# Optimization experiments

Measured on AMD Instinct MI355X. Metric: run time of the kernel, lower is better.

## Reference

```python
import math
import jax, jax.numpy as jnp
import numpy as np

B, S, D, H = 2, 2048, 1024, 16
HD = D // H

def setup_inputs() -> dict:
    key = jax.random.key(0)
    k1, k2, k3, k4, k5, k6 = jax.random.split(key, 6)
    q = jax.random.normal(k1, (B, S, D), dtype=jnp.float32)
    kv_mask = jax.random.bernoulli(k2, 0.95, (B, S))
    attn_mask = jax.random.bernoulli(k3, 0.95, (B, S, S))
    # nn.Linear(model_dim, 3*model_dim, bias=False): y = x @ W.T, W:[3D, D]
    W_all = jax.random.normal(k4, (3 * D, D), dtype=jnp.float32) / math.sqrt(D)
    W_out = jax.random.normal(k5, (D, D), dtype=jnp.float32) / math.sqrt(D)
    b_out = jax.random.normal(k6, (D,), dtype=jnp.float32) * 0.01
    return {"q": q, "kv_mask": kv_mask, "attn_mask": attn_mask,
            "W_all": W_all, "W_out": W_out, "b_out": b_out}

def reference(q, kv_mask, attn_mask, W_all, W_out, b_out):
    b, s, d = q.shape
    # merge_masks: kv_mask expanded over query dim, AND-ed with attn_mask, head dim added
    merged = (kv_mask[:, None, :] & attn_mask)[:, None, :, :]          # [b,1,s,s] bool
    # fused self-attn qkv projection
    qkv = q @ W_all.T                                                   # [b,s,3d]
    q_out, k_out, v_out = jnp.split(qkv, 3, axis=-1)
    reshape = lambda x: x.reshape(b, s, H, HD).transpose(0, 2, 1, 3)    # [b,h,s,hd]
    q_out, k_out, v_out = reshape(q_out), reshape(k_out), reshape(v_out)
    scores = jnp.einsum('bhqd,bhkd->bhqk', q_out, k_out) / math.sqrt(HD)
    scores = jnp.where(merged, scores, -jnp.inf)                        # masked_fill(~mask, -inf)
    att = jax.nn.softmax(scores, axis=-1)
    att = jnp.nan_to_num(att)                                           # fully-masked rows -> 0
    a_out = jnp.einsum('bhqk,bhkd->bhqd', att, v_out)
    a_out = a_out.transpose(0, 2, 1, 3).reshape(b, s, d)
    return a_out @ W_out.T + b_out
```

## Files before the change

kernel.cpp:

```cpp
#include <hip/hip_runtime.h>
#include <stdint.h>
#include <math.h>

namespace {

constexpr int kB  = 2;
constexpr int kS  = 2048;
constexpr int kD  = 1024;
constexpr int kH  = 16;
constexpr int kHD = 64;
constexpr int kBS = kB * kS;
constexpr int kD3 = 3 * kD;

typedef __attribute__((ext_vector_type(8)))  __bf16 bf16x8;
typedef __attribute__((ext_vector_type(4)))  float  f32x4;
typedef __attribute__((ext_vector_type(16))) float  f32x16;

__device__ __forceinline__ unsigned short f2bf(float f) {
  unsigned u = __float_as_uint(f);
  u += 0x7fffu + ((u >> 16) & 1u);
  return (unsigned short)(u >> 16);
}
__device__ __forceinline__ float bf2f(unsigned short b) {
  return __uint_as_float(((unsigned)b) << 16);
}
__device__ __forceinline__ unsigned pk2(float lo, float hi) {
  return (unsigned)f2bf(lo) | ((unsigned)f2bf(hi) << 16);
}
__device__ __forceinline__ unsigned cvtpk(float lo, float hi) {
  unsigned r;
  asm("v_cvt_pk_bf16_f32 %0, %1, %2" : "=v"(r) : "v"(lo), "v"(hi));
  return r;
}
__device__ __forceinline__ float max3f(float a, float b, float c) {
  float d;
  asm("v_max3_f32 %0, %1, %2, %3" : "=v"(d) : "v"(a), "v"(b), "v"(c));
  return d;
}
__device__ __forceinline__ void gload_lds16(const void* g, void* l) {
  __builtin_amdgcn_global_load_lds((const __attribute__((address_space(1))) void*)g,
                                   (__attribute__((address_space(3))) void*)l, 16, 0, 0);
}

__global__ __launch_bounds__(256) void cvt_kernel(const float* __restrict__ in,
                                                  unsigned short* __restrict__ out) {
  int i = blockIdx.x * 256 + threadIdx.x;
  float4 v = reinterpret_cast<const float4*>(in)[i];
  uint2 o;
  o.x = pk2(v.x, v.y);
  o.y = pk2(v.z, v.w);
  reinterpret_cast<uint2*>(out)[i] = o;
}

__global__ void detect_kernel(const unsigned* __restrict__ attn, unsigned* __restrict__ flag) {
  __shared__ int bad[4];
  unsigned v = attn[threadIdx.x];
  bool isbad = (v != 0u) && (v != 1u) && (v != 0x3f800000u);
  unsigned long long bal = __ballot(isbad);
  if ((threadIdx.x & 63) == 0) bad[threadIdx.x >> 6] = (bal != 0ull) ? 1 : 0;
  __syncthreads();
  if (threadIdx.x == 0) *flag = (bad[0] | bad[1] | bad[2] | bad[3]) ? 1u : 0u;
}

__global__ __launch_bounds__(256) void maskpack_kernel(const int* __restrict__ attn,
                                                       const int* __restrict__ kv,
                                                       const unsigned* __restrict__ flag,
                                                       unsigned* __restrict__ out) {
  int idx = blockIdx.x * 256 + threadIdx.x;
  int w = idx & 63;
  int q = (idx >> 6) & (kS - 1);
  int b = idx >> 17;
  unsigned m = 0;
  if (*flag == 0u) {
    const int* ap = attn + ((size_t)(b * kS + q)) * kS + w * 32;
    const int* kp = kv + b * kS + w * 32;
#pragma unroll
    for (int i = 0; i < 32; i++)
      if ((ap[i] != 0) & (kp[i] != 0)) m |= (1u << i);
  } else {
    const unsigned char* ap = (const unsigned char*)attn + ((size_t)(b * kS + q)) * kS + w * 32;
    const unsigned char* kp = (const unsigned char*)kv + b * kS + w * 32;
#pragma unroll
    for (int i = 0; i < 32; i++)
      if ((ap[i] != 0) & (kp[i] != 0)) m |= (1u << i);
  }
  out[idx] = m;
}

template <int OUT_BF16, int HAS_BIAS>
__global__ __launch_bounds__(256) void gemm_kernel(const unsigned short* __restrict__ A,
                                                   const unsigned short* __restrict__ Bt,
                                                   void* __restrict__ Cv,
                                                   const float* __restrict__ bias,
                                                   int M, int N, int K) {
  __shared__ alignas(16) unsigned short As[128 * 32];
  __shared__ alignas(16) unsigned short Bs[128 * 32];
  const int tid  = threadIdx.x;
  const int lane = tid & 63;
  const int wave = tid >> 6;
  const int wr = wave >> 1, wc = wave & 1;
  const int bm = blockIdx.x * 128;
  const int bn = blockIdx.y * 128;

  f32x4 acc[4][4] = {};

  const int srow  = tid >> 2;
  const int sslot = (tid & 3) ^ ((tid >> 3) & 3);
  const unsigned short* ga = A + (size_t)(bm + srow) * K + sslot * 8;
  const unsigned short* gb = Bt + (size_t)(bn + srow) * K + sslot * 8;
  unsigned short* lA = As + wave * 512;
  unsigned short* lB = Bs + wave * 512;

  for (int kk = 0; kk < K; kk += 32) {
    __syncthreads();
    gload_lds16(ga, lA);
    gload_lds16(ga + (size_t)64 * K, lA + 64 * 32);
    gload_lds16(gb, lB);
    gload_lds16(gb + (size_t)64 * K, lB + 64 * 32);
    ga += 32; gb += 32;
    __syncthreads();

    bf16x8 af[4], bfr[4];
#pragma unroll
    for (int i = 0; i < 4; i++) {
      int rA = wr * 64 + i * 16 + (lane & 15);
      int sA = (lane >> 4) ^ ((rA >> 1) & 3);
      af[i] = *(const bf16x8*)(As + rA * 32 + sA * 8);
      int rB = wc * 64 + i * 16 + (lane & 15);
      int sB = (lane >> 4) ^ ((rB >> 1) & 3);
      bfr[i] = *(const bf16x8*)(Bs + rB * 32 + sB * 8);
    }
#pragma unroll
    for (int mi = 0; mi < 4; mi++)
#pragma unroll
      for (int ni = 0; ni < 4; ni++)
        acc[mi][ni] = __builtin_amdgcn_mfma_f32_16x16x32_bf16(af[mi], bfr[ni], acc[mi][ni], 0, 0, 0);
  }

  const int r0 = bm + wr * 64 + (lane >> 4) * 4;
  const int c0 = bn + wc * 64 + (lane & 15);
#pragma unroll
  for (int ni = 0; ni < 4; ni++) {
    int c = c0 + ni * 16;
    float bv = HAS_BIAS ? bias[c] : 0.0f;
#pragma unroll
    for (int mi = 0; mi < 4; mi++) {
#pragma unroll
      for (int j = 0; j < 4; j++) {
        int r = r0 + mi * 16 + j;
        float v = acc[mi][ni][j] + bv;
        if (OUT_BF16) ((unsigned short*)Cv)[(size_t)r * N + c] = f2bf(v);
        else          ((float*)Cv)[(size_t)r * N + c] = v;
      }
    }
  }
}

__global__ __launch_bounds__(512, 2) void attn_kernel(const unsigned short* __restrict__ qkv,
                                                      const unsigned* __restrict__ maskp,
                                                      unsigned short* __restrict__ aout) {
  __shared__ alignas(16) unsigned short Ks[2][64 * 64];
  __shared__ alignas(16) unsigned short Vt[3][64 * 64];
  const int tid  = threadIdx.x;
  const int lane = tid & 63;
  const int wave = tid >> 6;
  const int half = lane >> 5;
  const int l31  = lane & 31;
  const int b = blockIdx.x >> 4;
  const int h = blockIdx.x & 15;
  const int qrow = blockIdx.y * 256 + wave * 32 + l31;
  const float NEGINF = -__builtin_inff();
  const float K2 = 1.4426950408889634f;

  bf16x8 qf[4];
  {
    const unsigned short* qp = qkv + (size_t)(b * kS + qrow) * kD3 + h * kHD + half * 8;
#pragma unroll
    for (int i = 0; i < 4; i++) {
      uint4 u = *(const uint4*)(qp + i * 16);
      unsigned w[4] = {u.x, u.y, u.z, u.w};
      union { unsigned u[4]; bf16x8 v; } o;
#pragma unroll
      for (int j = 0; j < 4; j++) {
        float lo = bf2f((unsigned short)(w[j] & 0xffffu)) * 0.125f;
        float hi = bf2f((unsigned short)(w[j] >> 16)) * 0.125f;
        o.u[j] = pk2(lo, hi);
      }
      qf[i] = o.v;
    }
  }

  f32x16 ot0 = {}, ot1 = {};
  float mrun = NEGINF, lrun = 0.f, m2 = 0.f;
  const unsigned* mp = maskp + ((size_t)(b * kS) + qrow) * 64;

  const int krow  = tid >> 3;
  const int kslot = (tid & 7) ^ (krow & 7);
  const unsigned short* gk = qkv + (size_t)(b * kS + krow) * kD3 + kD + h * kHD + kslot * 8;

  const int vp = tid >> 4;
  const int vo = (tid >> 1) & 7;
  const int vh = tid & 1;
  const unsigned short* gv = qkv + (size_t)(b * kS + 8 * vo + 4 * vh) * kD3 + 2 * kD + h * kHD + 2 * vp;
  const int vwo_lo = (2 * vp) * 128 + ((vo ^ ((2 * vp) & 7)) << 4) + vh * 8;
  const int vwo_hi = (2 * vp + 1) * 128 + ((vo ^ ((2 * vp + 1) & 7)) << 4) + vh * 8;

  const size_t tstride = (size_t)64 * kD3;

  gload_lds16(gk, (char*)Ks[0] + tid * 16);
  gload_lds16(gk + tstride, (char*)Ks[1] + tid * 16);
  {
    unsigned p0 = *(const unsigned*)(gv);
    unsigned p1 = *(const unsigned*)(gv + kD3);
    unsigned p2 = *(const unsigned*)(gv + 2 * kD3);
    unsigned p3 = *(const unsigned*)(gv + 3 * kD3);
    char* vb = (char*)Vt[0];
    uint2 wlo, whi;
    wlo.x = __builtin_amdgcn_perm(p1, p0, 0x05040100u);
    wlo.y = __builtin_amdgcn_perm(p3, p2, 0x05040100u);
    whi.x = __builtin_amdgcn_perm(p1, p0, 0x07060302u);
    whi.y = __builtin_amdgcn_perm(p3, p2, 0x07060302u);
    *(uint2*)(vb + vwo_lo) = wlo;
    *(uint2*)(vb + vwo_hi) = whi;
  }
  unsigned v0 = *(const unsigned*)(gv + tstride);
  unsigned v1 = *(const unsigned*)(gv + tstride + kD3);
  unsigned v2 = *(const unsigned*)(gv + tstride + 2 * kD3);
  unsigned v3 = *(const unsigned*)(gv + tstride + 3 * kD3);
  uint2 mw = *(const uint2*)(mp);
  __syncthreads();

  f32x16 sA0 = {}, sA1 = {}, sB0 = {}, sB1 = {};
  {
    const unsigned short* ksb = Ks[0];
    __builtin_amdgcn_s_setprio(1);
#pragma unroll
    for (int ii = 0; ii < 4; ii++) {
      int slot = (ii * 2 + half) ^ (l31 & 7);
      bf16x8 ka0 = *(const bf16x8*)(ksb + l31 * 64 + slot * 8);
      bf16x8 ka1 = *(const bf16x8*)(ksb + (l31 + 32) * 64 + slot * 8);
      sA0 = __builtin_amdgcn_mfma_f32_32x32x16_bf16(ka0, qf[ii], sA0, 0, 0, 0);
      sA1 = __builtin_amdgcn_mfma_f32_32x32x16_bf16(ka1, qf[ii], sA1, 0, 0, 0);
    }
    __builtin_amdgcn_s_setprio(0);
  }
  {
    char* vb = (char*)Vt[1];
    uint2 wlo, whi;
    wlo.x = __builtin_amdgcn_perm(v1, v0, 0x05040100u);
    wlo.y = __builtin_amdgcn_perm(v3, v2, 0x05040100u);
    whi.x = __builtin_amdgcn_perm(v1, v0, 0x07060302u);
    whi.y = __builtin_amdgcn_perm(v3, v2, 0x07060302u);
    *(uint2*)(vb + vwo_lo) = wlo;
    *(uint2*)(vb + vwo_hi) = whi;
  }
  __syncthreads();

  int vrd_off = 0;
  int vwr_off = 16384;

#define BODY(T, CUR0, CUR1, NXT0, NXT1, KNXT, KDST)                                         \
  {                                                                                         \
    const int t_ = (T);                                                                     \
    if (t_ < 31) {                                                                          \
      const unsigned short* ksb = (KNXT);                                                   \
      NXT0 = (f32x16){}; NXT1 = (f32x16){};                                                 \
      __builtin_amdgcn_s_setprio(1);                                                        \
      _Pragma("unroll")                                                                     \
      for (int ii = 0; ii < 4; ii++) {                                                      \
        int slot = (ii * 2 + half) ^ (l31 & 7);                                             \
        bf16x8 ka0 = *(const bf16x8*)(ksb + l31 * 64 + slot * 8);                           \
        bf16x8 ka1 = *(const bf16x8*)(ksb + (l31 + 32) * 64 + slot * 8);                    \
        NXT0 = __builtin_amdgcn_mfma_f32_32x32x16_bf16(ka0, qf[ii], NXT0, 0, 0, 0);         \
        NXT1 = __builtin_amdgcn_mfma_f32_32x32x16_bf16(ka1, qf[ii], NXT1, 0, 0, 0);         \
      }                                                                                     \
      __builtin_amdgcn_s_setprio(0);                                                        \
    }                                                                                       \
    __builtin_amdgcn_sched_barrier(0);                                                      \
    uint2 mwn = mw;                                                                         \
    if (t_ < 31) mwn = *(const uint2*)(mp + 2 * (t_ + 1));                                  \
    if (t_ < 30) {                                                                          \
      gload_lds16(gk + (size_t)(t_ + 2) * tstride, (KDST) + tid * 16);                      \
      const unsigned short* gvn = gv + (size_t)(t_ + 2) * tstride;                          \
      v0 = *(const unsigned*)(gvn);                                                         \
      v1 = *(const unsigned*)(gvn + kD3);                                                   \
      v2 = *(const unsigned*)(gvn + 2 * kD3);                                               \
      v3 = *(const unsigned*)(gvn + 3 * kD3);                                               \
    }                                                                                       \
    const unsigned mx = mw.x >> (4 * half);                                                 \
    const unsigned my = mw.y >> (4 * half);                                                 \
    float pm = NEGINF;                                                                      \
    _Pragma("unroll")                                                                       \
    for (int r = 0; r < 16; r++) pm = max3f(CUR0[r], CUR1[r], pm);                          \
    pm = fmaxf(pm, __shfl_xor(pm, 32));                                                     \
    if (__any(pm > mrun + 8.0f)) {                                                          \
      float mn = fmaxf(mrun, pm);                                                           \
      float m2n = mn * K2;                                                                  \
      float sc = __builtin_amdgcn_exp2f(fmaf(mrun, K2, -m2n));                              \
      m2 = m2n; mrun = mn; lrun *= sc;                                                      \
      _Pragma("unroll")                                                                     \
      for (int r = 0; r < 16; r++) { ot0[r] *= sc; ot1[r] *= sc; }                          \
    }                                                                                       \
    float ls0 = 0.f, ls1 = 0.f;                                                             \
    _Pragma("unroll")                                                                       \
    for (int r = 0; r < 16; r++) {                                                          \
      const int kb = (r & 3) + 8 * (r >> 2);                                                \
      float p0 = __builtin_amdgcn_exp2f(fmaf(CUR0[r], K2, -m2));                            \
      float p1 = __builtin_amdgcn_exp2f(fmaf(CUR1[r], K2, -m2));                            \
      unsigned z0 = (unsigned)__builtin_amdgcn_sbfe(mx, kb, 1);                             \
      unsigned z1 = (unsigned)__builtin_amdgcn_sbfe(my, kb, 1);                             \
      p0 = __uint_as_float(__float_as_uint(p0) & z0);                                       \
      p1 = __uint_as_float(__float_as_uint(p1) & z1);                                       \
      CUR0[r] = p0; CUR1[r] = p1;                                                           \
      ls0 += p0; ls1 += p1;                                                                 \
    }                                                                                       \
    float ls = ls0 + ls1;                                                                   \
    ls += __shfl_xor(ls, 32);                                                               \
    lrun += ls;                                                                             \
    const char* vtb = (const char*)Vt[0] + vrd_off;                                         \
    _Pragma("unroll")                                                                       \
    for (int gg = 0; gg < 2; gg++) {                                                        \
      unsigned w8[8];                                                                       \
      _Pragma("unroll")                                                                     \
      for (int j = 0; j < 8; j++)                                                           \
        w8[j] = gg ? cvtpk(CUR1[2 * j], CUR1[2 * j + 1])                                    \
                   : cvtpk(CUR0[2 * j], CUR0[2 * j + 1]);                                   \
      _Pragma("unroll")                                                                     \
      for (int cc = 0; cc < 2; cc++) {                                                      \
        unsigned u0 = w8[4 * cc],     u2 = w8[4 * cc + 2];                                  \
        unsigned u1 = w8[4 * cc + 1], u3 = w8[4 * cc + 3];                                  \
        asm("v_permlane32_swap_b32 %0, %1" : "+v"(u0), "+v"(u2));                           \
        asm("v_permlane32_swap_b32 %0, %1" : "+v"(u1), "+v"(u3));                           \
        union { unsigned u[4]; bf16x8 v; } pb;                                              \
        pb.u[0] = u0; pb.u[1] = u1; pb.u[2] = u2; pb.u[3] = u3;                             \
        int c = gg * 2 + cc;                                                                \
        int kslotc = (c * 2 + half) ^ (l31 & 7);                                            \
        __builtin_amdgcn_s_setprio(1);                                                      \
        {                                                                                   \
          bf16x8 va0 = *(const bf16x8*)(vtb + l31 * 128 + kslotc * 16);                     \
          bf16x8 va1 = *(const bf16x8*)(vtb + (l31 + 32) * 128 + kslotc * 16);              \
          ot0 = __builtin_amdgcn_mfma_f32_32x32x16_bf16(va0, pb.v, ot0, 0, 0, 0);           \
          ot1 = __builtin_amdgcn_mfma_f32_32x32x16_bf16(va1, pb.v, ot1, 0, 0, 0);           \
        }                                                                                   \
        __builtin_amdgcn_s_setprio(0);                                                      \
      }                                                                                     \
    }                                                                                       \
    if (t_ < 30) {                                                                          \
      char* vb = (char*)Vt[0] + vwr_off;                                                    \
      uint2 wlo, whi;                                                                       \
      wlo.x = __builtin_amdgcn_perm(v1, v0, 0x05040100u);                                   \
      wlo.y = __builtin_amdgcn_perm(v3, v2, 0x05040100u);                                   \
      whi.x = __builtin_amdgcn_perm(v1, v0, 0x07060302u);                                   \
      whi.y = __builtin_amdgcn_perm(v3, v2, 0x07060302u);                                   \
      *(uint2*)(vb + vwo_lo) = wlo;                                                         \
      *(uint2*)(vb + vwo_hi) = whi;                                                         \
    }                                                                                       \
    mw = mwn;                                                                               \
    vrd_off = (vrd_off == 16384) ? 0 : vrd_off + 8192;                                      \
    vwr_off = (vwr_off == 16384) ? 0 : vwr_off + 8192;                                      \
    __syncthreads();                                                                        \
  }

  for (int tp = 0; tp < 16; ++tp) {
    const int te = 2 * tp;
    BODY(te,     sA0, sA1, sB0, sB1, Ks[1], (char*)Ks[0]);
    BODY(te + 1, sB0, sB1, sA0, sA1, Ks[0], (char*)Ks[1]);
  }
#undef BODY

  float rl = (lrun > 0.f) ? (1.f / lrun) : 0.f;
  unsigned short* op = aout + (size_t)(b * kS + qrow) * kD + h * kHD;
#pragma unroll
  for (int hh = 0; hh < 2; hh++) {
#pragma unroll
    for (int qd = 0; qd < 4; qd++) {
      float x0 = (hh ? ot1[4 * qd]     : ot0[4 * qd])     * rl;
      float x1 = (hh ? ot1[4 * qd + 1] : ot0[4 * qd + 1]) * rl;
      float x2 = (hh ? ot1[4 * qd + 2] : ot0[4 * qd + 2]) * rl;
      float x3 = (hh ? ot1[4 * qd + 3] : ot0[4 * qd + 3]) * rl;
      uint2 o;
      o.x = pk2(x0, x1);
      o.y = pk2(x2, x3);
      *(uint2*)(op + hh * 32 + qd * 8 + half * 4) = o;
    }
  }
}

}

extern "C" void kernel_launch(void* const* d_in, const int* in_sizes, int n_in,
                              void* d_out, int out_size, void* d_ws, size_t ws_size,
                              hipStream_t stream) {
  (void)in_sizes; (void)n_in; (void)out_size; (void)ws_size;
  const float* q     = (const float*)d_in[0];
  const int*   kvm   = (const int*)d_in[1];
  const int*   am    = (const int*)d_in[2];
  const float* W_all = (const float*)d_in[3];
  const float* W_out = (const float*)d_in[4];
  const float* b_out = (const float*)d_in[5];

  char* ws = (char*)d_ws;
  unsigned short* qkv  = (unsigned short*)(ws);
  unsigned short* qbf  = (unsigned short*)(ws + 25165824);
  unsigned short* aout = qbf;
  unsigned short* wabf = (unsigned short*)(ws + 33554432);
  unsigned short* wobf = (unsigned short*)(ws + 39845888);
  unsigned*       mskp = (unsigned*)(ws + 41943040);
  unsigned*       flag = (unsigned*)(ws + 42991616);

  detect_kernel<<<1, 256, 0, stream>>>((const unsigned*)am, flag);
  maskpack_kernel<<<1024, 256, 0, stream>>>(am, kvm, flag, mskp);
  cvt_kernel<<<4096, 256, 0, stream>>>(q, qbf);
  cvt_kernel<<<3072, 256, 0, stream>>>(W_all, wabf);
  cvt_kernel<<<1024, 256, 0, stream>>>(W_out, wobf);
  gemm_kernel<1, 0><<<dim3(kBS / 128, kD3 / 128), 256, 0, stream>>>(qbf, wabf, qkv, nullptr, kBS, kD3, kD);
  attn_kernel<<<dim3(kB * kH, kS / 256), 512, 0, stream>>>(qkv, mskp, aout);
  gemm_kernel<0, 1><<<dim3(kBS / 128, kD / 128), 256, 0, stream>>>(aout, wobf, d_out, b_out, kBS, kD, kD);
}
```

Baseline: 159.4 us.

## Halve attention block to 256 threads and double per-thread K/V tile loads

Shrinks the attention workgroup from 8 to 4 waves (128 query rows per block) and doubles the grid, so each block covers its 64-row K/V tiles with half the threads. Each thread now issues two K async LDS loads and eight V dword loads per tile, writing both halves of the transposed V tile. The aim is more blocks in flight and cheaper barriers per block, at the cost of more global K/V traffic per query row and more registers per thread.

```diff
diff --git a/kernel.cpp b/kernel.cpp
--- a/kernel.cpp
+++ b/kernel.cpp
@@ -156,7 +156,7 @@
   }
 }
 
-__global__ __launch_bounds__(512, 2) void attn_kernel(const unsigned short* __restrict__ qkv,
+__global__ __launch_bounds__(256, 4) void attn_kernel(const unsigned short* __restrict__ qkv,
                                                       const unsigned* __restrict__ maskp,
                                                       unsigned short* __restrict__ aout) {
   __shared__ alignas(16) unsigned short Ks[2][64 * 64];
@@ -168,7 +168,7 @@
   const int l31  = lane & 31;
   const int b = blockIdx.x >> 4;
   const int h = blockIdx.x & 15;
-  const int qrow = blockIdx.y * 256 + wave * 32 + l31;
+  const int qrow = blockIdx.y * 128 + wave * 32 + l31;
   const float NEGINF = -__builtin_inff();
   const float K2 = 1.4426950408889634f;
 
@@ -207,26 +207,42 @@
 
   const size_t tstride = (size_t)64 * kD3;
 
+#define VLOAD8(PTR)                                        \
+    v0 = *(const unsigned*)(PTR);                          \
+    v1 = *(const unsigned*)((PTR) + kD3);                  \
+    v2 = *(const unsigned*)((PTR) + 2 * kD3);              \
+    v3 = *(const unsigned*)((PTR) + 3 * kD3);              \
+    v4 = *(const unsigned*)((PTR) + 32);                   \
+    v5 = *(const unsigned*)((PTR) + kD3 + 32);             \
+    v6 = *(const unsigned*)((PTR) + 2 * kD3 + 32);         \
+    v7 = *(const unsigned*)((PTR) + 3 * kD3 + 32);
+
+#define VWRITE(VB)                                                           \
+  {                                                                          \
+    char* vb_ = (VB);                                                        \
+    uint2 wlo, whi;                                                          \
+    wlo.x = __builtin_amdgcn_perm(v1, v0, 0x05040100u);                      \
+    wlo.y = __builtin_amdgcn_perm(v3, v2, 0x05040100u);                      \
+    whi.x = __builtin_amdgcn_perm(v1, v0, 0x07060302u);                      \
+    whi.y = __builtin_amdgcn_perm(v3, v2, 0x07060302u);                      \
+    *(uint2*)(vb_ + vwo_lo) = wlo;                                           \
+    *(uint2*)(vb_ + vwo_hi) = whi;                                           \
+    wlo.x = __builtin_amdgcn_perm(v5, v4, 0x05040100u);                      \
+    wlo.y = __builtin_amdgcn_perm(v7, v6, 0x05040100u);                      \
+    whi.x = __builtin_amdgcn_perm(v5, v4, 0x07060302u);                      \
+    whi.y = __builtin_amdgcn_perm(v7, v6, 0x07060302u);                      \
+    *(uint2*)(vb_ + 4096 + vwo_lo) = wlo;                                    \
+    *(uint2*)(vb_ + 4096 + vwo_hi) = whi;                                    \
+  }
+
+  unsigned v0, v1, v2, v3, v4, v5, v6, v7;
   gload_lds16(gk, (char*)Ks[0] + tid * 16);
+  gload_lds16(gk + 32 * kD3, (char*)Ks[0] + 4096 + tid * 16);
   gload_lds16(gk + tstride, (char*)Ks[1] + tid * 16);
-  {
-    unsigned p0 = *(const unsigned*)(gv);
-    unsigned p1 = *(const unsigned*)(gv + kD3);
-    unsigned p2 = *(const unsigned*)(gv + 2 * kD3);
-    unsigned p3 = *(const unsigned*)(gv + 3 * kD3);
-    char* vb = (char*)Vt[0];
-    uint2 wlo, whi;
-    wlo.x = __builtin_amdgcn_perm(p1, p0, 0x05040100u);
-    wlo.y = __builtin_amdgcn_perm(p3, p2, 0x05040100u);
-    whi.x = __builtin_amdgcn_perm(p1, p0, 0x07060302u);
-    whi.y = __builtin_amdgcn_perm(p3, p2, 0x07060302u);
-    *(uint2*)(vb + vwo_lo) = wlo;
-    *(uint2*)(vb + vwo_hi) = whi;
-  }
-  unsigned v0 = *(const unsigned*)(gv + tstride);
-  unsigned v1 = *(const unsigned*)(gv + tstride + kD3);
-  unsigned v2 = *(const unsigned*)(gv + tstride + 2 * kD3);
-  unsigned v3 = *(const unsigned*)(gv + tstride + 3 * kD3);
+  gload_lds16(gk + tstride + 32 * kD3, (char*)Ks[1] + 4096 + tid * 16);
+  VLOAD8(gv)
+  VWRITE((char*)Vt[0])
+  VLOAD8(gv + tstride)
   uint2 mw = *(const uint2*)(mp);
   __syncthreads();
 
@@ -244,16 +260,7 @@
     }
     __builtin_amdgcn_s_setprio(0);
   }
-  {
-    char* vb = (char*)Vt[1];
-    uint2 wlo, whi;
-    wlo.x = __builtin_amdgcn_perm(v1, v0, 0x05040100u);
-    wlo.y = __builtin_amdgcn_perm(v3, v2, 0x05040100u);
-    whi.x = __builtin_amdgcn_perm(v1, v0, 0x07060302u);
-    whi.y = __builtin_amdgcn_perm(v3, v2, 0x07060302u);
-    *(uint2*)(vb + vwo_lo) = wlo;
-    *(uint2*)(vb + vwo_hi) = whi;
-  }
+  VWRITE((char*)Vt[1])
   __syncthreads();
 
   int vrd_off = 0;
@@ -281,11 +288,9 @@
     if (t_ < 31) mwn = *(const uint2*)(mp + 2 * (t_ + 1));                                  \
     if (t_ < 30) {                                                                          \
       gload_lds16(gk + (size_t)(t_ + 2) * tstride, (KDST) + tid * 16);                      \
+      gload_lds16(gk + (size_t)(t_ + 2) * tstride + 32 * kD3, (KDST) + 4096 + tid * 16);    \
       const unsigned short* gvn = gv + (size_t)(t_ + 2) * tstride;                          \
-      v0 = *(const unsigned*)(gvn);                                                         \
-      v1 = *(const unsigned*)(gvn + kD3);                                                   \
-      v2 = *(const unsigned*)(gvn + 2 * kD3);                                               \
-      v3 = *(const unsigned*)(gvn + 3 * kD3);                                               \
+      VLOAD8(gvn)                                                                           \
     }                                                                                       \
     const unsigned mx = mw.x >> (4 * half);                                                 \
     const unsigned my = mw.y >> (4 * half);                                                 \
@@ -346,14 +351,7 @@
       }                                                                                     \
     }                                                                                       \
     if (t_ < 30) {                                                                          \
-      char* vb = (char*)Vt[0] + vwr_off;                                                    \
-      uint2 wlo, whi;                                                                       \
-      wlo.x = __builtin_amdgcn_perm(v1, v0, 0x05040100u);                                   \
-      wlo.y = __builtin_amdgcn_perm(v3, v2, 0x05040100u);                                   \
-      whi.x = __builtin_amdgcn_perm(v1, v0, 0x07060302u);                                   \
-      whi.y = __builtin_amdgcn_perm(v3, v2, 0x07060302u);                                   \
-      *(uint2*)(vb + vwo_lo) = wlo;                                                         \
-      *(uint2*)(vb + vwo_hi) = whi;                                                         \
+      VWRITE((char*)Vt[0] + vwr_off)                                                        \
     }                                                                                       \
     mw = mwn;                                                                               \
     vrd_off = (vrd_off == 16384) ? 0 : vrd_off + 8192;                                      \
@@ -367,6 +365,8 @@
     BODY(te + 1, sB0, sB1, sA0, sA1, Ks[0], (char*)Ks[1]);
   }
 #undef BODY
+#undef VLOAD8
+#undef VWRITE
 
   float rl = (lrun > 0.f) ? (1.f / lrun) : 0.f;
   unsigned short* op = aout + (size_t)(b * kS + qrow) * kD + h * kHD;
@@ -414,6 +414,6 @@
   cvt_kernel<<<3072, 256, 0, stream>>>(W_all, wabf);
   cvt_kernel<<<1024, 256, 0, stream>>>(W_out, wobf);
   gemm_kernel<1, 0><<<dim3(kBS / 128, kD3 / 128), 256, 0, stream>>>(qbf, wabf, qkv, nullptr, kBS, kD3, kD);
-  attn_kernel<<<dim3(kB * kH, kS / 256), 512, 0, stream>>>(qkv, mskp, aout);
+  attn_kernel<<<dim3(kB * kH, kS / 128), 256, 0, stream>>>(qkv, mskp, aout);
   gemm_kernel<0, 1><<<dim3(kBS / 128, kD / 128), 256, 0, stream>>>(aout, wobf, d_out, b_out, kBS, kD, kD);
 }
```

New measurement: 332.0 us. 2.08x slower.

## Deepen GEMM K-tile to 64 and fuse prep/detect kernels to cut launches

Applied to the files above, without the earlier changes.

The three float-to-bf16 conversion kernels are merged into a single prep kernel. The mask-format detection moves into each maskpack block, which drops two kernel launches and one global flag round-trip. The GEMM now stages a 128x64 K slice per iteration with an 8-slot XOR swizzle and performs two MFMAs per accumulator per sync, halving barrier count. This doubles LDS use per block and adds a launch_bounds occupancy hint. Every maskpack block now redundantly reads the first 256 mask words.

```diff
diff --git a/kernel.cpp b/kernel.cpp
--- a/kernel.cpp
+++ b/kernel.cpp
@@ -42,36 +42,46 @@
                                    (__attribute__((address_space(3))) void*)l, 16, 0, 0);
 }
 
-__global__ __launch_bounds__(256) void cvt_kernel(const float* __restrict__ in,
-                                                  unsigned short* __restrict__ out) {
-  int i = blockIdx.x * 256 + threadIdx.x;
-  float4 v = reinterpret_cast<const float4*>(in)[i];
+__global__ __launch_bounds__(256) void prep_kernel(const float* __restrict__ q,
+                                                   const float* __restrict__ Wa,
+                                                   const float* __restrict__ Wo,
+                                                   unsigned short* __restrict__ qb,
+                                                   unsigned short* __restrict__ wab,
+                                                   unsigned short* __restrict__ wob) {
+  int bx = blockIdx.x;
+  const float* src; unsigned short* dst; int base;
+  if (bx < 4096)      { src = q;  dst = qb;  base = 0; }
+  else if (bx < 7168) { src = Wa; dst = wab; base = 4096; }
+  else                { src = Wo; dst = wob; base = 7168; }
+  int i = (bx - base) * 256 + threadIdx.x;
+  float4 v = reinterpret_cast<const float4*>(src)[i];
   uint2 o;
   o.x = pk2(v.x, v.y);
   o.y = pk2(v.z, v.w);
-  reinterpret_cast<uint2*>(out)[i] = o;
-}
-
-__global__ void detect_kernel(const unsigned* __restrict__ attn, unsigned* __restrict__ flag) {
-  __shared__ int bad[4];
-  unsigned v = attn[threadIdx.x];
-  bool isbad = (v != 0u) && (v != 1u) && (v != 0x3f800000u);
-  unsigned long long bal = __ballot(isbad);
-  if ((threadIdx.x & 63) == 0) bad[threadIdx.x >> 6] = (bal != 0ull) ? 1 : 0;
-  __syncthreads();
-  if (threadIdx.x == 0) *flag = (bad[0] | bad[1] | bad[2] | bad[3]) ? 1u : 0u;
+  reinterpret_cast<uint2*>(dst)[i] = o;
 }
 
 __global__ __launch_bounds__(256) void maskpack_kernel(const int* __restrict__ attn,
                                                        const int* __restrict__ kv,
-                                                       const unsigned* __restrict__ flag,
                                                        unsigned* __restrict__ out) {
+  __shared__ int sflag;
+  {
+    unsigned v = ((const unsigned*)attn)[threadIdx.x];
+    bool isbad = (v != 0u) && (v != 1u) && (v != 0x3f800000u);
+    unsigned long long bal = __ballot(isbad);
+    if (threadIdx.x == 0) sflag = 0;
+    __syncthreads();
+    if ((threadIdx.x & 63) == 0 && bal != 0ull) sflag = 1;
+    __syncthreads();
+  }
+  const int flag = sflag;
+
   int idx = blockIdx.x * 256 + threadIdx.x;
   int w = idx & 63;
   int q = (idx >> 6) & (kS - 1);
   int b = idx >> 17;
   unsigned m = 0;
-  if (*flag == 0u) {
+  if (flag == 0) {
     const int* ap = attn + ((size_t)(b * kS + q)) * kS + w * 32;
     const int* kp = kv + b * kS + w * 32;
 #pragma unroll
@@ -88,13 +98,13 @@
 }
 
 template <int OUT_BF16, int HAS_BIAS>
-__global__ __launch_bounds__(256) void gemm_kernel(const unsigned short* __restrict__ A,
-                                                   const unsigned short* __restrict__ Bt,
-                                                   void* __restrict__ Cv,
-                                                   const float* __restrict__ bias,
-                                                   int M, int N, int K) {
-  __shared__ alignas(16) unsigned short As[128 * 32];
-  __shared__ alignas(16) unsigned short Bs[128 * 32];
+__global__ __launch_bounds__(256, 2) void gemm_kernel(const unsigned short* __restrict__ A,
+                                                      const unsigned short* __restrict__ Bt,
+                                                      void* __restrict__ Cv,
+                                                      const float* __restrict__ bias,
+                                                      int M, int N, int K) {
+  __shared__ alignas(16) unsigned short As[128 * 64];
+  __shared__ alignas(16) unsigned short Bs[128 * 64];
   const int tid  = threadIdx.x;
   const int lane = tid & 63;
   const int wave = tid >> 6;
@@ -104,37 +114,43 @@
 
   f32x4 acc[4][4] = {};
 
-  const int srow  = tid >> 2;
-  const int sslot = (tid & 3) ^ ((tid >> 3) & 3);
+  const int srow  = tid >> 3;
+  const int sslot = (tid & 7) ^ (srow & 7);
   const unsigned short* ga = A + (size_t)(bm + srow) * K + sslot * 8;
   const unsigned short* gb = Bt + (size_t)(bn + srow) * K + sslot * 8;
-  unsigned short* lA = As + wave * 512;
-  unsigned short* lB = Bs + wave * 512;
-
-  for (int kk = 0; kk < K; kk += 32) {
+  char* lA = (char*)As + wave * 1024;
+  char* lB = (char*)Bs + wave * 1024;
+
+  for (int kk = 0; kk < K; kk += 64) {
     __syncthreads();
-    gload_lds16(ga, lA);
-    gload_lds16(ga + (size_t)64 * K, lA + 64 * 32);
-    gload_lds16(gb, lB);
-    gload_lds16(gb + (size_t)64 * K, lB + 64 * 32);
-    ga += 32; gb += 32;
+#pragma unroll
+    for (int rb = 0; rb < 4; rb++) {
+      gload_lds16(ga + (size_t)(32 * rb) * K, lA + rb * 4096);
+      gload_lds16(gb + (size_t)(32 * rb) * K, lB + rb * 4096);
+    }
+    ga += 64; gb += 64;
     __syncthreads();
 
-    bf16x8 af[4], bfr[4];
+    bf16x8 af[4][2], bfr[4][2];
 #pragma unroll
     for (int i = 0; i < 4; i++) {
-      int rA = wr * 64 + i * 16 + (lane & 15);
-      int sA = (lane >> 4) ^ ((rA >> 1) & 3);
-      af[i] = *(const bf16x8*)(As + rA * 32 + sA * 8);
-      int rB = wc * 64 + i * 16 + (lane & 15);
-      int sB = (lane >> 4) ^ ((rB >> 1) & 3);
-      bfr[i] = *(const bf16x8*)(Bs + rB * 32 + sB * 8);
+#pragma unroll
+      for (int t = 0; t < 2; t++) {
+        int rA = wr * 64 + i * 16 + (lane & 15);
+        int jA = (t * 4 + (lane >> 4)) ^ (rA & 7);
+        af[i][t] = *(const bf16x8*)(As + rA * 64 + jA * 8);
+        int rB = wc * 64 + i * 16 + (lane & 15);
+        int jB = (t * 4 + (lane >> 4)) ^ (rB & 7);
+        bfr[i][t] = *(const bf16x8*)(Bs + rB * 64 + jB * 8);
+      }
     }
 #pragma unroll
     for (int mi = 0; mi < 4; mi++)
 #pragma unroll
-      for (int ni = 0; ni < 4; ni++)
-        acc[mi][ni] = __builtin_amdgcn_mfma_f32_16x16x32_bf16(af[mi], bfr[ni], acc[mi][ni], 0, 0, 0);
+      for (int ni = 0; ni < 4; ni++) {
+        acc[mi][ni] = __builtin_amdgcn_mfma_f32_16x16x32_bf16(af[mi][0], bfr[ni][0], acc[mi][ni], 0, 0, 0);
+        acc[mi][ni] = __builtin_amdgcn_mfma_f32_16x16x32_bf16(af[mi][1], bfr[ni][1], acc[mi][ni], 0, 0, 0);
+      }
   }
 
   const int r0 = bm + wr * 64 + (lane >> 4) * 4;
@@ -406,13 +422,9 @@
   unsigned short* wabf = (unsigned short*)(ws + 33554432);
   unsigned short* wobf = (unsigned short*)(ws + 39845888);
   unsigned*       mskp = (unsigned*)(ws + 41943040);
-  unsigned*       flag = (unsigned*)(ws + 42991616);
-
-  detect_kernel<<<1, 256, 0, stream>>>((const unsigned*)am, flag);
-  maskpack_kernel<<<1024, 256, 0, stream>>>(am, kvm, flag, mskp);
-  cvt_kernel<<<4096, 256, 0, stream>>>(q, qbf);
-  cvt_kernel<<<3072, 256, 0, stream>>>(W_all, wabf);
-  cvt_kernel<<<1024, 256, 0, stream>>>(W_out, wobf);
+
+  prep_kernel<<<8192, 256, 0, stream>>>(q, W_all, W_out, qbf, wabf, wobf);
+  maskpack_kernel<<<1024, 256, 0, stream>>>(am, kvm, mskp);
   gemm_kernel<1, 0><<<dim3(kBS / 128, kD3 / 128), 256, 0, stream>>>(qbf, wabf, qkv, nullptr, kBS, kD3, kD);
   attn_kernel<<<dim3(kB * kH, kS / 256), 512, 0, stream>>>(qkv, mskp, aout);
   gemm_kernel<0, 1><<<dim3(kBS / 128, kD / 128), 256, 0, stream>>>(aout, wobf, d_out, b_out, kBS, kD, kD);
```

Result: faster. 146.5 us (-8.1%).
